# Kernel tuning notes

Measured on AMD Instinct MI355X. Metric: run time of the kernel, lower is better.

The kernel has to match this reference:

```python
import jax, jax.numpy as jnp
import numpy as np


def setup_inputs() -> dict:
    key = jax.random.key(0)
    k1, k2, k3, k4, k5, k6 = jax.random.split(key, 6)
    B, I, H, O, A = 1024, 128, 512, 16, 8
    init_w = 0.003
    state = jax.random.normal(k1, (B, I), dtype=jnp.float32)
    action = jax.random.normal(k2, (B, A), dtype=jnp.float32)  # unused by forward (faithful to source)
    W1 = jax.random.uniform(k3, (O, I, H), dtype=jnp.float32, minval=-init_w, maxval=init_w)
    W2 = jax.random.uniform(k4, (O, H, H), dtype=jnp.float32, minval=-init_w, maxval=init_w)
    W3 = jax.random.uniform(k5, (O, H, 1), dtype=jnp.float32, minval=-init_w, maxval=init_w)
    option = jax.random.randint(k6, (B, 1), 0, O, dtype=jnp.int64)
    return {"state": state, "action": action, "W1": W1, "W2": W2, "W3": W3, "option": option}


def reference(state, action, W1, W2, W3, option):
    # option.long().flatten() -> per-sample weight gather, then chained batched matmuls.
    opt = option.astype(jnp.int32).reshape(-1)  # [B]
    x = jnp.einsum('bi,bih->bh', state, W1[opt])       # [B,1,I] @ [B,I,H]
    x = jnp.einsum('bh,bhk->bk', x, W2[opt])           # [B,1,H] @ [B,H,H]
    x = jnp.einsum('bh,bho->bo', x, W3[opt])           # [B,1,H] @ [B,H,1]
    return x.reshape(-1, 1)
```

## Files before the change

### kernel.cpp

```cpp
#include <hip/hip_runtime.h>

#define B_DIM 1024
#define I_DIM 128
#define H_DIM 512
#define O_CNT 16

__device__ __forceinline__ float wave_reduce_sum(float v) {
#pragma unroll
    for (int off = 32; off > 0; off >>= 1)
        v += __shfl_xor(v, off, 64);
    return v;
}

__global__ __launch_bounds__(256) void k_w2w3(const float* __restrict__ W2,
                                              const float* __restrict__ W3,
                                              float* __restrict__ u) {
    const int wid  = (blockIdx.x * 256 + threadIdx.x) >> 6;
    const int lane = threadIdx.x & 63;
    const int o = wid >> 9;
    const int h = wid & 511;
    const float4* row = (const float4*)(W2 + ((size_t)o * H_DIM + h) * H_DIM);
    const float4* w3  = (const float4*)(W3 + (size_t)o * H_DIM);
    float4 a0 = row[lane];
    float4 a1 = row[lane + 64];
    float4 b0 = w3[lane];
    float4 b1 = w3[lane + 64];
    float acc = a0.x * b0.x + a0.y * b0.y + a0.z * b0.z + a0.w * b0.w
              + a1.x * b1.x + a1.y * b1.y + a1.z * b1.z + a1.w * b1.w;
    acc = wave_reduce_sum(acc);
    if (lane == 0) u[wid] = acc;
}

__global__ __launch_bounds__(256) void k_w1u(const float* __restrict__ W1,
                                             const float* __restrict__ u,
                                             float* __restrict__ v) {
    const int wid  = (blockIdx.x * 256 + threadIdx.x) >> 6;
    const int lane = threadIdx.x & 63;
    const int o = wid >> 7;
    const int i = wid & 127;
    const float4* row = (const float4*)(W1 + ((size_t)o * I_DIM + i) * H_DIM);
    const float4* uo  = (const float4*)(u + (size_t)o * H_DIM);
    float4 a0 = row[lane];
    float4 a1 = row[lane + 64];
    float4 b0 = uo[lane];
    float4 b1 = uo[lane + 64];
    float acc = a0.x * b0.x + a0.y * b0.y + a0.z * b0.z + a0.w * b0.w
              + a1.x * b1.x + a1.y * b1.y + a1.z * b1.z + a1.w * b1.w;
    acc = wave_reduce_sum(acc);
    if (lane == 0) v[wid] = acc;
}

__global__ __launch_bounds__(256) void k_out(const float* __restrict__ state,
                                             const int* __restrict__ option,
                                             const float* __restrict__ v,
                                             float* __restrict__ out) {
    const int b    = (blockIdx.x * 256 + threadIdx.x) >> 6;
    const int lane = threadIdx.x & 63;
    const int o = option[b];
    const float2* srow = (const float2*)(state + (size_t)b * I_DIM);
    const float2* vrow = (const float2*)(v + (size_t)o * I_DIM);
    float2 s = srow[lane];
    float2 w = vrow[lane];
    float acc = s.x * w.x + s.y * w.y;
    acc = wave_reduce_sum(acc);
    if (lane == 0) out[b] = acc;
}

extern "C" void kernel_launch(void* const* d_in, const int* in_sizes, int n_in,
                              void* d_out, int out_size, void* d_ws, size_t ws_size,
                              hipStream_t stream) {
    const float* state  = (const float*)d_in[0];
    const float* W1     = (const float*)d_in[2];
    const float* W2     = (const float*)d_in[3];
    const float* W3     = (const float*)d_in[4];
    const int*   option = (const int*)d_in[5];
    float* out = (float*)d_out;

    float* u = (float*)d_ws;
    float* v = u + O_CNT * H_DIM;

    k_w2w3<<<2048, 256, 0, stream>>>(W2, W3, u);
    k_w1u<<<512, 256, 0, stream>>>(W1, u, v);
    k_out<<<256, 256, 0, stream>>>(state, option, v, out);
}
```

Baseline: 13.69 us.

## Fuse W1·u reduction and per-sample output into one per-option kernel

Merges the W1·u matvec and the final state·v dot product into a single kernel with one 1024-thread block per option. Each block computes its 128-entry v vector into shared memory, then scans all 1024 option indices and writes outputs only for samples that match its option. This saves one kernel launch and the global round trip for v. In exchange, only 16 blocks run, so most of the GPU sits idle, and every block reads the whole option array.

```diff
diff --git a/kernel.cpp b/kernel.cpp
--- a/kernel.cpp
+++ b/kernel.cpp
@@ -18,8 +18,7 @@
     const int wid  = (blockIdx.x * 256 + threadIdx.x) >> 6;
     const int lane = threadIdx.x & 63;
     const int o = wid >> 9;
-    const int h = wid & 511;
-    const float4* row = (const float4*)(W2 + ((size_t)o * H_DIM + h) * H_DIM);
+    const float4* row = (const float4*)(W2 + (size_t)wid * H_DIM);
     const float4* w3  = (const float4*)(W3 + (size_t)o * H_DIM);
     float4 a0 = row[lane];
     float4 a1 = row[lane + 64];
@@ -31,39 +30,49 @@
     if (lane == 0) u[wid] = acc;
 }
 
-__global__ __launch_bounds__(256) void k_w1u(const float* __restrict__ W1,
-                                             const float* __restrict__ u,
-                                             float* __restrict__ v) {
-    const int wid  = (blockIdx.x * 256 + threadIdx.x) >> 6;
-    const int lane = threadIdx.x & 63;
-    const int o = wid >> 7;
-    const int i = wid & 127;
-    const float4* row = (const float4*)(W1 + ((size_t)o * I_DIM + i) * H_DIM);
-    const float4* uo  = (const float4*)(u + (size_t)o * H_DIM);
-    float4 a0 = row[lane];
-    float4 a1 = row[lane + 64];
+__global__ __launch_bounds__(1024) void k_fused_vout(const float* __restrict__ W1,
+                                                     const float* __restrict__ u,
+                                                     const float* __restrict__ state,
+                                                     const int* __restrict__ option,
+                                                     float* __restrict__ out) {
+    const int o    = blockIdx.x;
+    const int tid  = threadIdx.x;
+    const int w    = tid >> 6;
+    const int lane = tid & 63;
+
+    __shared__ float v_s[I_DIM];
+    __shared__ int   opt_s[B_DIM];
+
+    opt_s[tid] = option[tid];
+
+    const float4* uo = (const float4*)(u + (size_t)o * H_DIM);
     float4 b0 = uo[lane];
     float4 b1 = uo[lane + 64];
-    float acc = a0.x * b0.x + a0.y * b0.y + a0.z * b0.z + a0.w * b0.w
-              + a1.x * b1.x + a1.y * b1.y + a1.z * b1.z + a1.w * b1.w;
-    acc = wave_reduce_sum(acc);
-    if (lane == 0) v[wid] = acc;
-}
 
-__global__ __launch_bounds__(256) void k_out(const float* __restrict__ state,
-                                             const int* __restrict__ option,
-                                             const float* __restrict__ v,
-                                             float* __restrict__ out) {
-    const int b    = (blockIdx.x * 256 + threadIdx.x) >> 6;
-    const int lane = threadIdx.x & 63;
-    const int o = option[b];
-    const float2* srow = (const float2*)(state + (size_t)b * I_DIM);
-    const float2* vrow = (const float2*)(v + (size_t)o * I_DIM);
-    float2 s = srow[lane];
-    float2 w = vrow[lane];
-    float acc = s.x * w.x + s.y * w.y;
-    acc = wave_reduce_sum(acc);
-    if (lane == 0) out[b] = acc;
+#pragma unroll
+    for (int r = 0; r < 8; ++r) {
+        const int i = w * 8 + r;
+        const float4* row = (const float4*)(W1 + ((size_t)o * I_DIM + i) * H_DIM);
+        float4 a0 = row[lane];
+        float4 a1 = row[lane + 64];
+        float acc = a0.x * b0.x + a0.y * b0.y + a0.z * b0.z + a0.w * b0.w
+                  + a1.x * b1.x + a1.y * b1.y + a1.z * b1.z + a1.w * b1.w;
+        acc = wave_reduce_sum(acc);
+        if (lane == 0) v_s[i] = acc;
+    }
+    __syncthreads();
+
+    const float2 vv = *(const float2*)(v_s + 2 * lane);
+    for (int t = 0; t < B_DIM / 16; ++t) {
+        const int b = w + (t << 4);
+        if (opt_s[b] == o) {
+            const float2* srow = (const float2*)(state + (size_t)b * I_DIM);
+            float2 s = srow[lane];
+            float acc = s.x * vv.x + s.y * vv.y;
+            acc = wave_reduce_sum(acc);
+            if (lane == 0) out[b] = acc;
+        }
+    }
 }
 
 extern "C" void kernel_launch(void* const* d_in, const int* in_sizes, int n_in,
@@ -77,9 +86,7 @@
     float* out = (float*)d_out;
 
     float* u = (float*)d_ws;
-    float* v = u + O_CNT * H_DIM;
 
     k_w2w3<<<2048, 256, 0, stream>>>(W2, W3, u);
-    k_w1u<<<512, 256, 0, stream>>>(W1, u, v);
-    k_out<<<256, 256, 0, stream>>>(state, option, v, out);
+    k_fused_vout<<<O_CNT, 1024, 0, stream>>>(W1, u, state, option, out);
 }
```

Result: slower. 19.81 us (+44.7%).

## Merge W2·W3 reduction with per-option state·W1 pass into one launch

Applied to the files above, without the earlier changes.

Replaces the three-kernel chain (W2·W3, W1·u, state·v) with two launches. The first kernel runs the W2·W3 reduction alongside blocks that compute state·W1[o] for the samples grouped by option and write a full 1024x512 intermediate. A second kernel dots that intermediate with u. This removes one launch and its dependency, but adds a 2 MB intermediate write and read, serial option scanning, and a heavier per-sample matmul than the precollapsed v path.

```diff
diff --git a/kernel.cpp b/kernel.cpp
--- a/kernel.cpp
+++ b/kernel.cpp
@@ -4,6 +4,8 @@
 #define I_DIM 128
 #define H_DIM 512
 #define O_CNT 16
+#define S1_BLOCKS 256
+#define U_BLOCKS  2048
 
 __device__ __forceinline__ float wave_reduce_sum(float v) {
 #pragma unroll
@@ -12,21 +14,107 @@
     return v;
 }
 
+__global__ __launch_bounds__(256) void k_phase1(const float* __restrict__ W1,
+                                                const float* __restrict__ W2,
+                                                const float* __restrict__ W3,
+                                                const float* __restrict__ state,
+                                                const int* __restrict__ option,
+                                                float* __restrict__ u,
+                                                float* __restrict__ s1)
+{
+    const int bid = blockIdx.x;
+    const int tid = threadIdx.x;
+
+    if (bid >= S1_BLOCKS) {
+        const int wid  = ((bid - S1_BLOCKS) << 2) + (tid >> 6);
+        const int lane = tid & 63;
+        const int o    = wid >> 9;
+        const float4* row = (const float4*)(W2 + (size_t)wid * H_DIM);
+        const float4* w3  = (const float4*)(W3 + (size_t)o * H_DIM);
+        float4 a0 = row[lane], a1 = row[lane + 64];
+        float4 b0 = w3[lane],  b1 = w3[lane + 64];
+        float acc = a0.x*b0.x + a0.y*b0.y + a0.z*b0.z + a0.w*b0.w
+                  + a1.x*b1.x + a1.y*b1.y + a1.z*b1.z + a1.w*b1.w;
+        acc = wave_reduce_sum(acc);
+        if (lane == 0) u[wid] = acc;
+        return;
+    }
+
+    const int o    = bid >> 4;
+    const int base = (bid & 15) << 6;
+    const float2* W1o = (const float2*)(W1 + (size_t)o * I_DIM * H_DIM);
+    float2* s1p = (float2*)s1;
+
+    int g0 = 0, g1 = 0, g2 = 0, g3 = 0, cnt = 0;
+
+    auto flush = [&](int n) {
+        const int b0 = g0;
+        const int b1 = (n > 1) ? g1 : g0;
+        const int b2 = (n > 2) ? g2 : g0;
+        const int b3 = (n > 3) ? g3 : g0;
+        const float* st0 = state + (size_t)b0 * I_DIM;
+        const float* st1 = state + (size_t)b1 * I_DIM;
+        const float* st2 = state + (size_t)b2 * I_DIM;
+        const float* st3 = state + (size_t)b3 * I_DIM;
+        float2 a0 = {0.f, 0.f}, a1 = a0, a2 = a0, a3 = a0;
+#pragma unroll 4
+        for (int i = 0; i < I_DIM; ++i) {
+            float2 w = W1o[(size_t)i * (H_DIM / 2) + tid];
+            float v0 = st0[i], v1 = st1[i], v2 = st2[i], v3 = st3[i];
+            a0.x += v0 * w.x; a0.y += v0 * w.y;
+            a1.x += v1 * w.x; a1.y += v1 * w.y;
+            a2.x += v2 * w.x; a2.y += v2 * w.y;
+            a3.x += v3 * w.x; a3.y += v3 * w.y;
+        }
+        s1p[(size_t)b0 * (H_DIM / 2) + tid] = a0;
+        if (n > 1) s1p[(size_t)b1 * (H_DIM / 2) + tid] = a1;
+        if (n > 2) s1p[(size_t)b2 * (H_DIM / 2) + tid] = a2;
+        if (n > 3) s1p[(size_t)b3 * (H_DIM / 2) + tid] = a3;
+    };
+
+    for (int t = 0; t < 64; ++t) {
+        if (option[base + t] == o) {
+            const int b = base + t;
+            g0 = (cnt == 0) ? b : g0;
+            g1 = (cnt == 1) ? b : g1;
+            g2 = (cnt == 2) ? b : g2;
+            g3 = (cnt == 3) ? b : g3;
+            if (++cnt == 4) { flush(4); cnt = 0; }
+        }
+    }
+    if (cnt > 0) flush(cnt);
+}
+
+__global__ __launch_bounds__(256) void k_out2(const float* __restrict__ s1,
+                                              const float* __restrict__ u,
+                                              const int* __restrict__ option,
+                                              float* __restrict__ out)
+{
+    const int b    = (blockIdx.x * 256 + threadIdx.x) >> 6;
+    const int lane = threadIdx.x & 63;
+    const int o    = option[b];
+    const float4* xr = (const float4*)(s1 + (size_t)b * H_DIM);
+    const float4* ur = (const float4*)(u + (size_t)o * H_DIM);
+    float4 x0 = xr[lane], x1 = xr[lane + 64];
+    float4 u0 = ur[lane], u1 = ur[lane + 64];
+    float acc = x0.x*u0.x + x0.y*u0.y + x0.z*u0.z + x0.w*u0.w
+              + x1.x*u1.x + x1.y*u1.y + x1.z*u1.z + x1.w*u1.w;
+    acc = wave_reduce_sum(acc);
+    if (lane == 0) out[b] = acc;
+}
+
 __global__ __launch_bounds__(256) void k_w2w3(const float* __restrict__ W2,
                                               const float* __restrict__ W3,
                                               float* __restrict__ u) {
     const int wid  = (blockIdx.x * 256 + threadIdx.x) >> 6;
     const int lane = threadIdx.x & 63;
     const int o = wid >> 9;
-    const int h = wid & 511;
-    const float4* row = (const float4*)(W2 + ((size_t)o * H_DIM + h) * H_DIM);
+    const float4* row = (const float4*)(W2 + (size_t)wid * H_DIM);
     const float4* w3  = (const float4*)(W3 + (size_t)o * H_DIM);
-    float4 a0 = row[lane];
-    float4 a1 = row[lane + 64];
-    float4 b0 = w3[lane];
-    float4 b1 = w3[lane + 64];
-    float acc = a0.x * b0.x + a0.y * b0.y + a0.z * b0.z + a0.w * b0.w
-              + a1.x * b1.x + a1.y * b1.y + a1.z * b1.z + a1.w * b1.w;
+    float4 a0 = row[lane], a1 = row[lane + 64];
+    float4 b0 = w3[lane],  b1 = w3[lane + 64];
+    float acc = a0.x*b0.x + a0.y*b0.y + a0.z*b0.z + a0.w*b0.w
+              + a1.x*b1.x + a1.y*b1.y + a1.z*b1.z + a1.w*b1.w;
     acc = wave_reduce_sum(acc);
     if (lane == 0) u[wid] = acc;
 }
@@ -37,15 +125,12 @@
     const int wid  = (blockIdx.x * 256 + threadIdx.x) >> 6;
     const int lane = threadIdx.x & 63;
     const int o = wid >> 7;
-    const int i = wid & 127;
-    const float4* row = (const float4*)(W1 + ((size_t)o * I_DIM + i) * H_DIM);
+    const float4* row = (const float4*)(W1 + (size_t)wid * H_DIM);
     const float4* uo  = (const float4*)(u + (size_t)o * H_DIM);
-    float4 a0 = row[lane];
-    float4 a1 = row[lane + 64];
-    float4 b0 = uo[lane];
-    float4 b1 = uo[lane + 64];
-    float acc = a0.x * b0.x + a0.y * b0.y + a0.z * b0.z + a0.w * b0.w
-              + a1.x * b1.x + a1.y * b1.y + a1.z * b1.z + a1.w * b1.w;
+    float4 a0 = row[lane], a1 = row[lane + 64];
+    float4 b0 = uo[lane],  b1 = uo[lane + 64];
+    float acc = a0.x*b0.x + a0.y*b0.y + a0.z*b0.z + a0.w*b0.w
+              + a1.x*b1.x + a1.y*b1.y + a1.z*b1.z + a1.w*b1.w;
     acc = wave_reduce_sum(acc);
     if (lane == 0) v[wid] = acc;
 }
@@ -77,9 +162,17 @@
     float* out = (float*)d_out;
 
     float* u = (float*)d_ws;
-    float* v = u + O_CNT * H_DIM;
+    const size_t need = (size_t)(O_CNT * H_DIM) * 4
+                      + (size_t)B_DIM * H_DIM * 4;
 
-    k_w2w3<<<2048, 256, 0, stream>>>(W2, W3, u);
-    k_w1u<<<512, 256, 0, stream>>>(W1, u, v);
-    k_out<<<256, 256, 0, stream>>>(state, option, v, out);
+    if (ws_size >= need) {
+        float* s1 = u + O_CNT * H_DIM;
+        k_phase1<<<S1_BLOCKS + U_BLOCKS, 256, 0, stream>>>(W1, W2, W3, state, option, u, s1);
+        k_out2<<<B_DIM / 4, 256, 0, stream>>>(s1, u, option, out);
+    } else {
+        float* v = u + O_CNT * H_DIM;
+        k_w2w3<<<2048, 256, 0, stream>>>(W2, W3, u);
+        k_w1u<<<512, 256, 0, stream>>>(W1, u, v);
+        k_out<<<256, 256, 0, stream>>>(state, option, v, out);
+    }
 }
```

Result: slower. 34.04 us (+148.7%).

## Fuse weight-chain reductions into one chunked kernel plus partial-sum reduce

Applied to the files above, without the earlier changes.

Replaces the three dependent kernels with one fused kernel. Each block owns an option and a 16-row chunk of H: it computes that slice of W2·W3, folds it into W1 to get a partial projection vector, and writes per-sample partial outputs only for the samples whose option matches. A second small kernel sums the 32 chunk partials per sample. This removes a kernel launch and the global round trips through the u and v buffers. In exchange it adds a partial-sum buffer, ballot-driven serial loops over matching samples, and a fallback path used when the workspace is too small.

```diff
diff --git a/kernel.cpp b/kernel.cpp
--- a/kernel.cpp
+++ b/kernel.cpp
@@ -4,6 +4,8 @@
 #define I_DIM 128
 #define H_DIM 512
 #define O_CNT 16
+#define NCHUNK 32
+#define CH 16
 
 __device__ __forceinline__ float wave_reduce_sum(float v) {
 #pragma unroll
@@ -12,44 +14,114 @@
     return v;
 }
 
+__global__ __launch_bounds__(256) void k_fused(const float* __restrict__ W1,
+                                               const float* __restrict__ W2,
+                                               const float* __restrict__ W3,
+                                               const float* __restrict__ state,
+                                               const int* __restrict__ option,
+                                               float* __restrict__ partial)
+{
+    const int o    = blockIdx.x >> 5;
+    const int c    = blockIdx.x & 31;
+    const int tid  = threadIdx.x;
+    const int w    = tid >> 6;
+    const int lane = tid & 63;
+
+    __shared__ float u_s[CH];
+    __shared__ float y_s[I_DIM];
+    __shared__ int   opt_s[B_DIM];
+
+#pragma unroll
+    for (int g = 0; g < 4; ++g) opt_s[tid + 256 * g] = option[tid + 256 * g];
+
+    const float4* w3 = (const float4*)(W3 + (size_t)o * H_DIM);
+    const float4 b0 = w3[lane], b1 = w3[lane + 64];
+#pragma unroll
+    for (int j = 0; j < 4; ++j) {
+        const int r = w * 4 + j;
+        const int h = c * CH + r;
+        const float4* rp = (const float4*)(W2 + ((size_t)o * H_DIM + h) * H_DIM);
+        float4 a0 = rp[lane], a1 = rp[lane + 64];
+        float acc = a0.x*b0.x + a0.y*b0.y + a0.z*b0.z + a0.w*b0.w
+                  + a1.x*b1.x + a1.y*b1.y + a1.z*b1.z + a1.w*b1.w;
+        acc = wave_reduce_sum(acc);
+        if (lane == 0) u_s[r] = acc;
+    }
+    __syncthreads();
+
+    if (tid < I_DIM) {
+        const float4* wp = (const float4*)(W1 + ((size_t)o * I_DIM + tid) * H_DIM + c * CH);
+        float y = 0.f;
+#pragma unroll
+        for (int q = 0; q < 4; ++q) {
+            float4 wv = wp[q];
+            y += wv.x * u_s[q*4+0] + wv.y * u_s[q*4+1]
+               + wv.z * u_s[q*4+2] + wv.w * u_s[q*4+3];
+        }
+        y_s[tid] = y;
+    }
+    __syncthreads();
+
+    const float2 yv = *(const float2*)(y_s + 2 * lane);
+#pragma unroll
+    for (int g = 0; g < 4; ++g) {
+        const int bbase = w * 256 + g * 64;
+        const int m = opt_s[bbase + lane];
+        unsigned long long mask = __ballot(m == o);
+        while (mask) {
+            const int bit = __ffsll((long long)mask) - 1;
+            mask &= mask - 1;
+            const int b = bbase + bit;
+            const float2* sr = (const float2*)(state + (size_t)b * I_DIM);
+            float2 s = sr[lane];
+            float acc = s.x * yv.x + s.y * yv.y;
+            acc = wave_reduce_sum(acc);
+            if (lane == 0) partial[(size_t)c * B_DIM + b] = acc;
+        }
+    }
+}
+
+__global__ __launch_bounds__(256) void k_reduce(const float* __restrict__ partial,
+                                                float* __restrict__ out)
+{
+    const int b = blockIdx.x * 256 + threadIdx.x;
+    float acc = 0.f;
+#pragma unroll
+    for (int c = 0; c < NCHUNK; ++c)
+        acc += partial[(size_t)c * B_DIM + b];
+    out[b] = acc;
+}
+
 __global__ __launch_bounds__(256) void k_w2w3(const float* __restrict__ W2,
                                               const float* __restrict__ W3,
                                               float* __restrict__ u) {
     const int wid  = (blockIdx.x * 256 + threadIdx.x) >> 6;
     const int lane = threadIdx.x & 63;
     const int o = wid >> 9;
-    const int h = wid & 511;
-    const float4* row = (const float4*)(W2 + ((size_t)o * H_DIM + h) * H_DIM);
+    const float4* row = (const float4*)(W2 + (size_t)wid * H_DIM);
     const float4* w3  = (const float4*)(W3 + (size_t)o * H_DIM);
-    float4 a0 = row[lane];
-    float4 a1 = row[lane + 64];
-    float4 b0 = w3[lane];
-    float4 b1 = w3[lane + 64];
-    float acc = a0.x * b0.x + a0.y * b0.y + a0.z * b0.z + a0.w * b0.w
-              + a1.x * b1.x + a1.y * b1.y + a1.z * b1.z + a1.w * b1.w;
+    float4 a0 = row[lane], a1 = row[lane + 64];
+    float4 b0 = w3[lane],  b1 = w3[lane + 64];
+    float acc = a0.x*b0.x + a0.y*b0.y + a0.z*b0.z + a0.w*b0.w
+              + a1.x*b1.x + a1.y*b1.y + a1.z*b1.z + a1.w*b1.w;
     acc = wave_reduce_sum(acc);
     if (lane == 0) u[wid] = acc;
 }
-
 __global__ __launch_bounds__(256) void k_w1u(const float* __restrict__ W1,
                                              const float* __restrict__ u,
                                              float* __restrict__ v) {
     const int wid  = (blockIdx.x * 256 + threadIdx.x) >> 6;
     const int lane = threadIdx.x & 63;
     const int o = wid >> 7;
-    const int i = wid & 127;
-    const float4* row = (const float4*)(W1 + ((size_t)o * I_DIM + i) * H_DIM);
+    const float4* row = (const float4*)(W1 + (size_t)wid * H_DIM);
     const float4* uo  = (const float4*)(u + (size_t)o * H_DIM);
-    float4 a0 = row[lane];
-    float4 a1 = row[lane + 64];
-    float4 b0 = uo[lane];
-    float4 b1 = uo[lane + 64];
-    float acc = a0.x * b0.x + a0.y * b0.y + a0.z * b0.z + a0.w * b0.w
-              + a1.x * b1.x + a1.y * b1.y + a1.z * b1.z + a1.w * b1.w;
+    float4 a0 = row[lane], a1 = row[lane + 64];
+    float4 b0 = uo[lane],  b1 = uo[lane + 64];
+    float acc = a0.x*b0.x + a0.y*b0.y + a0.z*b0.z + a0.w*b0.w
+              + a1.x*b1.x + a1.y*b1.y + a1.z*b1.z + a1.w*b1.w;
     acc = wave_reduce_sum(acc);
     if (lane == 0) v[wid] = acc;
 }
-
 __global__ __launch_bounds__(256) void k_out(const float* __restrict__ state,
                                              const int* __restrict__ option,
                                              const float* __restrict__ v,
@@ -76,10 +148,17 @@
     const int*   option = (const int*)d_in[5];
     float* out = (float*)d_out;
 
-    float* u = (float*)d_ws;
-    float* v = u + O_CNT * H_DIM;
+    const size_t need = (size_t)NCHUNK * B_DIM * sizeof(float);
 
-    k_w2w3<<<2048, 256, 0, stream>>>(W2, W3, u);
-    k_w1u<<<512, 256, 0, stream>>>(W1, u, v);
-    k_out<<<256, 256, 0, stream>>>(state, option, v, out);
+    if (ws_size >= need) {
+        float* partial = (float*)d_ws;
+        k_fused<<<O_CNT * NCHUNK, 256, 0, stream>>>(W1, W2, W3, state, option, partial);
+        k_reduce<<<B_DIM / 256, 256, 0, stream>>>(partial, out);
+    } else {
+        float* u = (float*)d_ws;
+        float* v = u + O_CNT * H_DIM;
+        k_w2w3<<<2048, 256, 0, stream>>>(W2, W3, u);
+        k_w1u<<<512, 256, 0, stream>>>(W1, u, v);
+        k_out<<<256, 256, 0, stream>>>(state, option, v, out);
+    }
 }
```

Result: slower. 18.20 us (+33.0%).
